# Performance work log

Measured on AMD Instinct MI355X. Metric: run time of the kernel, lower is better.

Reference implementation:

```python
import jax, jax.numpy as jnp
import numpy as np
import math

D_MODEL = 2048
N_HEADS = 16
D_K = D_MODEL // N_HEADS


def setup_inputs() -> dict:
    key = jax.random.key(0)
    ks = jax.random.split(key, 10)
    B, S = 1, 2048
    scale = 1.0 / math.sqrt(D_MODEL)
    x = jax.random.normal(ks[0], (B, S, D_MODEL), dtype=jnp.float32)
    mask = jnp.ones((1, 1, S, S), dtype=bool)
    Wq = jax.random.normal(ks[1], (D_MODEL, D_MODEL), dtype=jnp.float32) * scale
    bq = jnp.zeros((D_MODEL,), dtype=jnp.float32)
    Wk = jax.random.normal(ks[2], (D_MODEL, D_MODEL), dtype=jnp.float32) * scale
    bk = jnp.zeros((D_MODEL,), dtype=jnp.float32)
    Wv = jax.random.normal(ks[3], (D_MODEL, D_MODEL), dtype=jnp.float32) * scale
    bv = jnp.zeros((D_MODEL,), dtype=jnp.float32)
    Wo = jax.random.normal(ks[4], (D_MODEL, D_MODEL), dtype=jnp.float32) * scale
    bo = jnp.zeros((D_MODEL,), dtype=jnp.float32)
    return {"x": x, "mask": mask, "Wq": Wq, "bq": bq, "Wk": Wk, "bk": bk,
            "Wv": Wv, "bv": bv, "Wo": Wo, "bo": bo}


def reference(x, mask, Wq, bq, Wk, bk, Wv, bv, Wo, bo):
    B, S, D = x.shape
    # projections (nn.Linear: y = x @ W.T + b; here W stored as [in, out] so x @ W + b)
    def proj(W, b):
        y = x @ W + b                                   # [B, S, D]
        return y.reshape(B, S, N_HEADS, D_K).transpose(0, 2, 1, 3)  # [B, H, S, d_k]
    Q = proj(Wq, bq)
    K = proj(Wk, bk)
    V = proj(Wv, bv)
    scores = jnp.einsum('bhqd,bhkd->bhqk', Q, K) / math.sqrt(D_K)  # [B, H, S, S]
    scores = jnp.where(mask, scores, -jnp.inf)
    attn = jax.nn.softmax(scores, axis=-1)
    out = jnp.einsum('bhqk,bhkd->bhqd', attn, V)        # [B, H, S, d_k]
    out = out.transpose(0, 2, 1, 3).reshape(B, S, D)    # [B, S, D]
    return out @ Wo + bo
```

## Files before the change

kernel.cpp:

```cpp
#include <hip/hip_runtime.h>
#include <cstdint>
#include <cstddef>

typedef __bf16 bf16;
typedef bf16 bf16x8 __attribute__((ext_vector_type(8)));
typedef bf16 bf16x4 __attribute__((ext_vector_type(4)));
typedef bf16 bf16x2 __attribute__((ext_vector_type(2)));
typedef float f32x4 __attribute__((ext_vector_type(4)));
typedef float f32x16 __attribute__((ext_vector_type(16)));
typedef uint32_t u32x4 __attribute__((ext_vector_type(4)));

#define AS1 __attribute__((address_space(1)))
#define AS3 __attribute__((address_space(3)))

constexpr int DMODEL = 2048;
constexpr int SEQ    = 2048;
constexpr int DK     = 128;
constexpr float QSCALE_LOG2E = 0.12751740f;
constexpr float SM_SHIFT = 12.0f;

__global__ __launch_bounds__(256) void prep_kernel(
    const float* __restrict__ x, bf16* __restrict__ xb,
    const float* __restrict__ W0, const float* __restrict__ W1,
    const float* __restrict__ W2, const float* __restrict__ W3,
    bf16* __restrict__ T0, bf16* __restrict__ T1,
    bf16* __restrict__ T2, bf16* __restrict__ T3) {
  int bx = blockIdx.x;
  int tid = threadIdx.x;
  if (bx < 2048) {
    size_t i = (size_t)bx * 256 + tid;
    const float4 a = ((const float4*)x)[i * 2];
    const float4 b = ((const float4*)x)[i * 2 + 1];
    bf16x8 v;
    v[0] = (bf16)a.x; v[1] = (bf16)a.y; v[2] = (bf16)a.z; v[3] = (bf16)a.w;
    v[4] = (bf16)b.x; v[5] = (bf16)b.y; v[6] = (bf16)b.z; v[7] = (bf16)b.w;
    *(bf16x8*)(xb + i * 8) = v;
    return;
  }
  int b2 = bx - 2048;
  int z = b2 >> 10;
  int t = b2 & 1023;
  int bi = t >> 5, bj = t & 31;
  const float* W = (z == 0) ? W0 : (z == 1) ? W1 : (z == 2) ? W2 : W3;
  bf16* T        = (z == 0) ? T0 : (z == 1) ? T1 : (z == 2) ? T2 : T3;

  __shared__ float tile[64][68];
  int tr = tid >> 4, tc = tid & 15;
#pragma unroll
  for (int i = 0; i < 4; i++) {
    float4 v = *(const float4*)(W + (size_t)(bi * 64 + tr + i * 16) * DMODEL + bj * 64 + tc * 4);
    *(float4*)&tile[tr + i * 16][tc * 4] = v;
  }
  __syncthreads();
  int nl = tid >> 2, kc = (tid & 3) * 16;
  bf16x8 o0, o1;
#pragma unroll
  for (int j = 0; j < 8; j++) {
    o0[j] = (bf16)tile[kc + j][nl];
    o1[j] = (bf16)tile[kc + 8 + j][nl];
  }
  bf16* dst = T + (size_t)(bj * 64 + nl) * DMODEL + bi * 64 + kc;
  *(bf16x8*)dst       = o0;
  *(bf16x8*)(dst + 8) = o1;
}

__global__ __launch_bounds__(512, 2) void gemm256_qkv_kernel(
    const bf16* __restrict__ A,
    const bf16* __restrict__ Bt0, const float* __restrict__ bias0, bf16* __restrict__ outQ,
    const bf16* __restrict__ Bt1, const float* __restrict__ bias1, bf16* __restrict__ outK,
    const bf16* __restrict__ Bt2, const float* __restrict__ bias2, bf16* __restrict__ outV) {
  constexpr int NT = DMODEL / 64;
  __shared__ bf16 Asl[2][16384];
  __shared__ bf16 Bsl[2][16384];

  int zt = blockIdx.x >> 6;
  int t  = blockIdx.x & 63;
  int tm = t >> 3, tn = t & 7;
  int m0 = tm * 256, n0 = tn * 256;
  const bf16* Btp   = (zt == 0) ? Bt0 : (zt == 1) ? Bt1 : Bt2;
  const float* bias = (zt == 0) ? bias0 : (zt == 1) ? bias1 : bias2;

  int tid = threadIdx.x;
  int w = tid >> 6, l = tid & 63;
  int wm = w >> 2, wn = w & 3;
  int g = l >> 4, r16 = l & 15;

  int u0 = tid, u1 = 512 + tid;
  int r0 = u0 >> 3, s0 = u0 & 7;
  int r1 = u1 >> 3, s1 = u1 & 7;
  const bf16* aS0 = A + (size_t)(m0 + r0) * DMODEL + (s0 ^ (r0 & 7)) * 8;
  const bf16* aS1 = A + (size_t)(m0 + r1) * DMODEL + (s1 ^ (r1 & 7)) * 8;
  const bf16* bS0 = Btp + (size_t)(n0 + r0) * DMODEL + (s0 ^ (r0 & 7)) * 8;
  const bf16* bS1 = Btp + (size_t)(n0 + r1) * DMODEL + (s1 ^ (r1 & 7)) * 8;

  auto STAGE = [&](int tile, int h) {
    if (tile >= NT) return;
    int buf = tile & 1;
    size_t roff = (size_t)(h & 1) * 128 * DMODEL + (size_t)tile * 64;
    if (h < 2) {
      __builtin_amdgcn_global_load_lds((const AS1 void*)(aS0 + roff),
          (AS3 void*)(&Asl[buf][(h & 1) * 8192 + u0 * 8]), 16, 0, 0);
      __builtin_amdgcn_global_load_lds((const AS1 void*)(aS1 + roff),
          (AS3 void*)(&Asl[buf][(h & 1) * 8192 + u1 * 8]), 16, 0, 0);
    } else {
      __builtin_amdgcn_global_load_lds((const AS1 void*)(bS0 + roff),
          (AS3 void*)(&Bsl[buf][(h & 1) * 8192 + u0 * 8]), 16, 0, 0);
      __builtin_amdgcn_global_load_lds((const AS1 void*)(bS1 + roff),
          (AS3 void*)(&Bsl[buf][(h & 1) * 8192 + u1 * 8]), 16, 0, 0);
    }
  };

  bf16x8 afq[2][8];
  bf16x8 bfn[2][4];
  f32x4 acc[8][4];
#pragma unroll
  for (int i = 0; i < 8; i++)
#pragma unroll
    for (int j = 0; j < 4; j++) acc[i][j] = (f32x4){0.f, 0.f, 0.f, 0.f};

#define G256_LDA(MQ, BUF)                                                      \
  _Pragma("unroll")                                                            \
  for (int mf = 0; mf < 4; mf++) {                                             \
    int row = wm * 128 + (MQ) * 64 + mf * 16 + r16;                            \
    _Pragma("unroll")                                                          \
    for (int ks = 0; ks < 2; ks++)                                             \
      afq[MQ][mf * 2 + ks] =                                                   \
          *(const bf16x8*)(&Asl[BUF][row * 64 + (((ks * 4 + g) ^ (row & 7)) * 8)]); \
  }
#define G256_LDB(NQ, BUF)                                                      \
  _Pragma("unroll")                                                            \
  for (int nf = 0; nf < 2; nf++) {                                             \
    int row = wn * 64 + (NQ) * 32 + nf * 16 + r16;                             \
    _Pragma("unroll")                                                          \
    for (int ks = 0; ks < 2; ks++)                                             \
      bfn[NQ][nf * 2 + ks] =                                                   \
          *(const bf16x8*)(&Bsl[BUF][row * 64 + (((ks * 4 + g) ^ (row & 7)) * 8)]); \
  }
#define G256_MMA(MQ, NQ)                                                       \
  _Pragma("unroll")                                                            \
  for (int ks = 0; ks < 2; ks++)                                               \
    _Pragma("unroll")                                                          \
    for (int mf = 0; mf < 4; mf++)                                             \
      _Pragma("unroll")                                                        \
      for (int nf = 0; nf < 2; nf++)                                           \
        acc[(MQ) * 4 + mf][(NQ) * 2 + nf] =                                    \
            __builtin_amdgcn_mfma_f32_16x16x32_bf16(afq[MQ][mf * 2 + ks],      \
                bfn[NQ][nf * 2 + ks], acc[(MQ) * 4 + mf][(NQ) * 2 + nf], 0, 0, 0);
#define G256_BAR() __builtin_amdgcn_s_barrier()
#define G256_P1()  __builtin_amdgcn_s_setprio(1)
#define G256_P0()  __builtin_amdgcn_s_setprio(0)

  STAGE(0, 0); STAGE(0, 1); STAGE(0, 2); STAGE(0, 3);
  STAGE(1, 0); STAGE(1, 1); STAGE(1, 2);
  asm volatile("s_waitcnt vmcnt(6)" ::: "memory");
  G256_BAR();

  for (int it = 0; it < NT / 2; ++it) {
    int t1 = 2 * it + 1, t2 = 2 * it + 2, t3 = 2 * it + 3;
    G256_LDA(0, 0) G256_LDB(0, 0)
    STAGE(t1, 3);
    G256_BAR(); G256_P1(); G256_MMA(0, 0) G256_P0(); G256_BAR();
    G256_LDA(1, 0)
    STAGE(t2, 0);
    G256_BAR(); G256_P1(); G256_MMA(1, 0) G256_P0(); G256_BAR();
    G256_LDB(1, 0)
    STAGE(t2, 1);
    G256_BAR(); G256_P1(); G256_MMA(1, 1) G256_P0(); G256_BAR();
    STAGE(t2, 2);
    G256_BAR(); G256_P1(); G256_MMA(0, 1) G256_P0();
    if (it < NT / 2 - 1) asm volatile("s_waitcnt vmcnt(6)" ::: "memory");
    else                 asm volatile("s_waitcnt vmcnt(0)" ::: "memory");
    G256_BAR();
    G256_LDA(0, 1) G256_LDB(0, 1)
    STAGE(t2, 3);
    G256_BAR(); G256_P1(); G256_MMA(0, 0) G256_P0(); G256_BAR();
    G256_LDA(1, 1)
    STAGE(t3, 0);
    G256_BAR(); G256_P1(); G256_MMA(1, 0) G256_P0(); G256_BAR();
    G256_LDB(1, 1)
    STAGE(t3, 1);
    G256_BAR(); G256_P1(); G256_MMA(1, 1) G256_P0(); G256_BAR();
    STAGE(t3, 2);
    G256_BAR(); G256_P1(); G256_MMA(0, 1) G256_P0();
    if (it < NT / 2 - 1) asm volatile("s_waitcnt vmcnt(6)" ::: "memory");
    G256_BAR();
  }

  float bval[4];
#pragma unroll
  for (int nf = 0; nf < 4; nf++) bval[nf] = bias[n0 + wn * 64 + nf * 16 + r16];

  if (zt == 2) {
#pragma unroll
    for (int mf = 0; mf < 8; mf++)
#pragma unroll
      for (int nf = 0; nf < 4; nf++) {
        bf16x4 pk;
#pragma unroll
        for (int r = 0; r < 4; r++) pk[r] = (bf16)(acc[mf][nf][r] + bval[nf]);
        *(bf16x4*)(outV + (size_t)(n0 + wn * 64 + nf * 16 + r16) * SEQ +
                   m0 + wm * 128 + mf * 16 + g * 4) = pk;
      }
  } else {
    bf16* outp = (zt == 0) ? outQ : outK;
    float scl  = (zt == 0) ? QSCALE_LOG2E : 1.0f;
#pragma unroll
    for (int mf = 0; mf < 8; mf++)
#pragma unroll
      for (int nf = 0; nf < 4; nf++)
#pragma unroll
        for (int r = 0; r < 4; r++)
          outp[(size_t)(m0 + wm * 128 + mf * 16 + g * 4 + r) * DMODEL +
               n0 + wn * 64 + nf * 16 + r16] =
              (bf16)((acc[mf][nf][r] + bval[nf]) * scl);
  }
#undef G256_LDA
#undef G256_LDB
#undef G256_MMA
#undef G256_BAR
#undef G256_P1
#undef G256_P0
}

__global__ __launch_bounds__(256, 2) void attn_kernel(const bf16* __restrict__ Q,
                                                      const bf16* __restrict__ K,
                                                      const bf16* __restrict__ Vt,
                                                      bf16* __restrict__ Opart,
                                                      float* __restrict__ Lp) {
  constexpr int NT = 1024 / 64;
  int bx = blockIdx.x;
  int qt = bx >> 5;
  int hh = bx & 31;
  int h = hh >> 1, half = hh & 1;
  int tid = threadIdx.x;
  int w = tid >> 6, l = tid & 63;
  int q5 = l & 31, h5 = l >> 5;

  __shared__ bf16 KL[2][8192];
  __shared__ bf16 VL[2][8192];

  int q0 = qt * 128 + w * 32;

  const bf16* ksrc[4];
  const bf16* vsrc[4];
#pragma unroll
  for (int i = 0; i < 4; i++) {
    int unit = i * 256 + tid;
    ksrc[i] = K  + (size_t)(half * 1024 + (unit & 63)) * DMODEL + h * DK + (unit >> 6) * 8;
    vsrc[i] = Vt + (size_t)(h * DK + (unit & 127)) * SEQ + half * 1024 + (unit >> 7) * 8;
  }

#define ATTN_STAGE(BUF)                                                        \
  {                                                                            \
    _Pragma("unroll")                                                          \
    for (int i_ = 0; i_ < 4; i_++) {                                           \
      __builtin_amdgcn_global_load_lds((const AS1 void*)ksrc[i_],              \
          (AS3 void*)(&KL[BUF][(i_ * 256 + tid) * 8]), 16, 0, 0);              \
      ksrc[i_] += 64 * DMODEL;                                                 \
      __builtin_amdgcn_global_load_lds((const AS1 void*)vsrc[i_],              \
          (AS3 void*)(&VL[BUF][(i_ * 256 + tid) * 8]), 16, 0, 0);              \
      vsrc[i_] += 64;                                                          \
    }                                                                          \
  }

  bf16x8 qb[8];
  {
    const bf16* qbase = Q + (size_t)(q0 + q5) * DMODEL + h * DK + h5 * 8;
#pragma unroll
    for (int kc = 0; kc < 8; kc++) qb[kc] = *(const bf16x8*)(qbase + kc * 16);
  }

  f32x16 o[4];
#pragma unroll
  for (int vf = 0; vf < 4; vf++)
#pragma unroll
    for (int i = 0; i < 16; i++) o[vf][i] = 0.f;
  float lrow = 0.f;

  ATTN_STAGE(0);
  __syncthreads();

  for (int kb = 0; kb < NT; kb++) {
    int cur = kb & 1;
    if (kb + 1 < NT) ATTN_STAGE(cur ^ 1);

    const bf16* KB = &KL[cur][0];
    f32x16 s0, s1;
#pragma unroll
    for (int i = 0; i < 16; i++) { s0[i] = 0.f; s1[i] = 0.f; }
#pragma unroll
    for (int kc = 0; kc < 8; kc++) {
      bf16x8 k0 = *(const bf16x8*)(KB + ((kc * 2 + h5) * 64 + q5) * 8);
      bf16x8 k1 = *(const bf16x8*)(KB + ((kc * 2 + h5) * 64 + 32 + q5) * 8);
      s0 = __builtin_amdgcn_mfma_f32_32x32x16_bf16(k0, qb[kc], s0, 0, 0, 0);
      s1 = __builtin_amdgcn_mfma_f32_32x32x16_bf16(k1, qb[kc], s1, 0, 0, 0);
    }

#pragma unroll
    for (int i = 0; i < 16; i++) s0[i] = exp2f(s0[i] - SM_SHIFT);
#pragma unroll
    for (int i = 0; i < 16; i++) s1[i] = exp2f(s1[i] - SM_SHIFT);
    float ta[8];
#pragma unroll
    for (int i = 0; i < 8; i++) ta[i] = (s0[i] + s0[i + 8]) + (s1[i] + s1[i + 8]);
#pragma unroll
    for (int i = 0; i < 4; i++) ta[i] += ta[i + 4];
    float ps = (ta[0] + ta[2]) + (ta[1] + ta[3]);
    ps += __shfl_xor(ps, 32);
    lrow += ps;

    uint32_t u[16];
#pragma unroll
    for (int rp = 0; rp < 8; rp++) {
      bf16x2 t0; t0[0] = (bf16)s0[2 * rp]; t0[1] = (bf16)s0[2 * rp + 1];
      u[rp] = __builtin_bit_cast(uint32_t, t0);
      bf16x2 t1; t1[0] = (bf16)s1[2 * rp]; t1[1] = (bf16)s1[2 * rp + 1];
      u[8 + rp] = __builtin_bit_cast(uint32_t, t1);
    }
#pragma unroll
    for (int b = 0; b < 16; b += 4) {
      asm volatile("v_permlane32_swap_b32 %0, %1" : "+v"(u[b]),     "+v"(u[b + 2]));
      asm volatile("v_permlane32_swap_b32 %0, %1" : "+v"(u[b + 1]), "+v"(u[b + 3]));
    }

    const bf16* VB = &VL[cur][0];
#pragma unroll
    for (int ks = 0; ks < 4; ks++) {
      u32x4 tw = {u[ks * 4], u[ks * 4 + 1], u[ks * 4 + 2], u[ks * 4 + 3]};
      bf16x8 pb = __builtin_bit_cast(bf16x8, tw);
#pragma unroll
      for (int vf = 0; vf < 4; vf++) {
        bf16x8 vv = *(const bf16x8*)(VB + ((ks * 2 + h5) * 128 + vf * 32 + q5) * 8);
        o[vf] = __builtin_amdgcn_mfma_f32_32x32x16_bf16(vv, pb, o[vf], 0, 0, 0);
      }
    }
    __syncthreads();
  }

  bf16* obase = Opart + ((size_t)hh * SEQ + q0 + q5) * DK + h5 * 4;
#pragma unroll
  for (int vf = 0; vf < 4; vf++)
#pragma unroll
    for (int rr = 0; rr < 4; rr++) {
      bf16x4 pk;
#pragma unroll
      for (int c = 0; c < 4; c++) pk[c] = (bf16)o[vf][rr * 4 + c];
      *(bf16x4*)(obase + vf * 32 + rr * 8) = pk;
    }
  if (h5 == 0) Lp[(size_t)hh * SEQ + q0 + q5] = lrow;
#undef ATTN_STAGE
}

__global__ __launch_bounds__(256) void attn_merge_kernel(const bf16* __restrict__ Opart,
                                                         const float* __restrict__ Lp,
                                                         bf16* __restrict__ AO) {
  size_t idx = (size_t)blockIdx.x * 256 + threadIdx.x;
  int d8 = idx & 15;
  int q  = (int)((idx >> 4) & 2047);
  int h  = (int)(idx >> 15);
  size_t ra = (size_t)(h * 2) * SEQ + q;
  size_t rb = (size_t)(h * 2 + 1) * SEQ + q;
  float inv = 1.0f / (Lp[ra] + Lp[rb]);
  bf16x8 a = *(const bf16x8*)(Opart + ra * DK + d8 * 8);
  bf16x8 b = *(const bf16x8*)(Opart + rb * DK + d8 * 8);
  bf16x8 r;
#pragma unroll
  for (int j = 0; j < 8; j++)
    r[j] = (bf16)(((float)a[j] + (float)b[j]) * inv);
  *(bf16x8*)(AO + (size_t)q * DMODEL + h * DK + d8 * 8) = r;
}

__global__ __launch_bounds__(256) void gemm_bt_kernel(
    const bf16* __restrict__ A,
    const bf16* __restrict__ Btp, const float* __restrict__ bias,
    float* __restrict__ outF) {
  __shared__ bf16 Als[128 * 64];
  __shared__ bf16 Bls[128 * 64];

  int t = blockIdx.x;
  int tm = t >> 4, tn = t & 15;
  int m0 = tm * 128, n0 = tn * 128;
  int tid = threadIdx.x;
  int w = tid >> 6, l = tid & 63;
  int wm = w >> 1, wn = w & 1;
  int g = l >> 4, r16 = l & 15;

  f32x4 acc[4][4];
#pragma unroll
  for (int i = 0; i < 4; i++)
#pragma unroll
    for (int j = 0; j < 4; j++) acc[i][j] = (f32x4){0.f, 0.f, 0.f, 0.f};

  int lrow = l >> 3;
  for (int kt = 0; kt < DMODEL / 64; kt++) {
    const bf16* abase = A   + (size_t)m0 * DMODEL + kt * 64;
    const bf16* bbase = Btp + (size_t)n0 * DMODEL + kt * 64;
#pragma unroll
    for (int i = 0; i < 4; i++) {
      int chunk = w * 4 + i;
      int row   = chunk * 8 + lrow;
      int slot  = (l & 7) ^ (row & 7);
      __builtin_amdgcn_global_load_lds((const AS1 void*)(abase + (size_t)row * DMODEL + slot * 8),
                                       (AS3 void*)(Als + chunk * 512), 16, 0, 0);
      __builtin_amdgcn_global_load_lds((const AS1 void*)(bbase + (size_t)row * DMODEL + slot * 8),
                                       (AS3 void*)(Bls + chunk * 512), 16, 0, 0);
    }
    __syncthreads();
#pragma unroll
    for (int ks = 0; ks < 2; ks++) {
      bf16x8 af[4], bfr[4];
#pragma unroll
      for (int mf = 0; mf < 4; mf++) {
        int row  = wm * 64 + mf * 16 + r16;
        int slot = (ks * 4 + g) ^ (row & 7);
        af[mf] = *(const bf16x8*)(Als + row * 64 + slot * 8);
      }
#pragma unroll
      for (int nf = 0; nf < 4; nf++) {
        int row  = wn * 64 + nf * 16 + r16;
        int slot = (ks * 4 + g) ^ (row & 7);
        bfr[nf] = *(const bf16x8*)(Bls + row * 64 + slot * 8);
      }
#pragma unroll
      for (int mf = 0; mf < 4; mf++)
#pragma unroll
        for (int nf = 0; nf < 4; nf++)
          acc[mf][nf] = __builtin_amdgcn_mfma_f32_16x16x32_bf16(af[mf], bfr[nf], acc[mf][nf], 0, 0, 0);
    }
    __syncthreads();
  }

  float bval[4];
#pragma unroll
  for (int nf = 0; nf < 4; nf++) bval[nf] = bias[n0 + wn * 64 + nf * 16 + r16];
#pragma unroll
  for (int mf = 0; mf < 4; mf++)
#pragma unroll
    for (int nf = 0; nf < 4; nf++)
#pragma unroll
      for (int r = 0; r < 4; r++)
        outF[(size_t)(m0 + wm * 64 + mf * 16 + g * 4 + r) * DMODEL + n0 + wn * 64 + nf * 16 + r16] =
            acc[mf][nf][r] + bval[nf];
}

extern "C" void kernel_launch(void* const* d_in, const int* in_sizes, int n_in,
                              void* d_out, int out_size, void* d_ws, size_t ws_size,
                              hipStream_t stream) {
  const float* x  = (const float*)d_in[0];
  const float* Wq = (const float*)d_in[2];
  const float* bq = (const float*)d_in[3];
  const float* Wk = (const float*)d_in[4];
  const float* bk = (const float*)d_in[5];
  const float* Wv = (const float*)d_in[6];
  const float* bv = (const float*)d_in[7];
  const float* Wo = (const float*)d_in[8];
  const float* bo = (const float*)d_in[9];
  float* out = (float*)d_out;

  const size_t MAT = (size_t)DMODEL * DMODEL;
  bf16* p   = (bf16*)d_ws;
  bf16* xb  = p; p += MAT;
  bf16* Wqt = p; p += MAT;
  bf16* Wkt = p; p += MAT;
  bf16* Wvt = p; p += MAT;
  bf16* Wot = p; p += MAT;
  bf16* Qb  = p; p += MAT;
  bf16* Kb  = p; p += MAT;
  bf16* Vtb = p; p += MAT;
  bf16* AOb = p; p += MAT;
  bf16* Opart  = xb;
  float* Lpart = (float*)p;

  prep_kernel<<<6144, 256, 0, stream>>>(x, xb, Wq, Wk, Wv, Wo, Wqt, Wkt, Wvt, Wot);
  gemm256_qkv_kernel<<<192, 512, 0, stream>>>(xb, Wqt, bq, Qb, Wkt, bk, Kb, Wvt, bv, Vtb);
  attn_kernel<<<512, 256, 0, stream>>>(Qb, Kb, Vtb, Opart, Lpart);
  attn_merge_kernel<<<2048, 256, 0, stream>>>(Opart, Lpart, AOb);
  gemm_bt_kernel<<<256, 256, 0, stream>>>(AOb, Wot, bo, out);
}
```

Measured before the change: 182.9 us.

## Fuse QKV projections into one GEMM with 256x192 tiles over concatenated weights

Replaces the three-way z-split QKV GEMM (192 blocks of 256x256) with a single GEMM over the concatenated transposed Q/K/V weights (N=6144), tiled 256x192, giving 256 blocks. That count fills the 256 CUs evenly in one wave, where 192 blocks left some idle. The load and MMA schedule is rebuilt for the narrower B tile, and the epilogue picks the bias and output per column. It relies on Wqt/Wkt/Wvt sitting contiguously in the workspace, which the layout provides, and the new vmcnt waits must match the changed load counts.

```diff
diff --git a/kernel.cpp b/kernel.cpp
--- a/kernel.cpp
+++ b/kernel.cpp
@@ -64,21 +64,18 @@
   *(bf16x8*)(dst + 8) = o1;
 }
 
-__global__ __launch_bounds__(512, 2) void gemm256_qkv_kernel(
+__global__ __launch_bounds__(512, 2) void gemm_qkv_fused_kernel(
     const bf16* __restrict__ A,
-    const bf16* __restrict__ Bt0, const float* __restrict__ bias0, bf16* __restrict__ outQ,
-    const bf16* __restrict__ Bt1, const float* __restrict__ bias1, bf16* __restrict__ outK,
-    const bf16* __restrict__ Bt2, const float* __restrict__ bias2, bf16* __restrict__ outV) {
+    const bf16* __restrict__ BtF,
+    const float* __restrict__ bias0, const float* __restrict__ bias1,
+    const float* __restrict__ bias2,
+    bf16* __restrict__ outQ, bf16* __restrict__ outK, bf16* __restrict__ outV) {
   constexpr int NT = DMODEL / 64;
   __shared__ bf16 Asl[2][16384];
-  __shared__ bf16 Bsl[2][16384];
-
-  int zt = blockIdx.x >> 6;
-  int t  = blockIdx.x & 63;
-  int tm = t >> 3, tn = t & 7;
-  int m0 = tm * 256, n0 = tn * 256;
-  const bf16* Btp   = (zt == 0) ? Bt0 : (zt == 1) ? Bt1 : Bt2;
-  const float* bias = (zt == 0) ? bias0 : (zt == 1) ? bias1 : bias2;
+  __shared__ bf16 Bsl[2][12288];
+
+  int tm = blockIdx.x >> 5, tn = blockIdx.x & 31;
+  int m0 = tm * 256, n0 = tn * 192;
 
   int tid = threadIdx.x;
   int w = tid >> 6, l = tid & 63;
@@ -90,35 +87,35 @@
   int r1 = u1 >> 3, s1 = u1 & 7;
   const bf16* aS0 = A + (size_t)(m0 + r0) * DMODEL + (s0 ^ (r0 & 7)) * 8;
   const bf16* aS1 = A + (size_t)(m0 + r1) * DMODEL + (s1 ^ (r1 & 7)) * 8;
-  const bf16* bS0 = Btp + (size_t)(n0 + r0) * DMODEL + (s0 ^ (r0 & 7)) * 8;
-  const bf16* bS1 = Btp + (size_t)(n0 + r1) * DMODEL + (s1 ^ (r1 & 7)) * 8;
-
-  auto STAGE = [&](int tile, int h) {
+  int br = tid >> 3, bs = tid & 7;
+  const bf16* bS = BtF + (size_t)(n0 + br) * DMODEL + (bs ^ (br & 7)) * 8;
+
+  auto STAGE_A = [&](int tile, int h) {
     if (tile >= NT) return;
     int buf = tile & 1;
-    size_t roff = (size_t)(h & 1) * 128 * DMODEL + (size_t)tile * 64;
-    if (h < 2) {
-      __builtin_amdgcn_global_load_lds((const AS1 void*)(aS0 + roff),
-          (AS3 void*)(&Asl[buf][(h & 1) * 8192 + u0 * 8]), 16, 0, 0);
-      __builtin_amdgcn_global_load_lds((const AS1 void*)(aS1 + roff),
-          (AS3 void*)(&Asl[buf][(h & 1) * 8192 + u1 * 8]), 16, 0, 0);
-    } else {
-      __builtin_amdgcn_global_load_lds((const AS1 void*)(bS0 + roff),
-          (AS3 void*)(&Bsl[buf][(h & 1) * 8192 + u0 * 8]), 16, 0, 0);
-      __builtin_amdgcn_global_load_lds((const AS1 void*)(bS1 + roff),
-          (AS3 void*)(&Bsl[buf][(h & 1) * 8192 + u1 * 8]), 16, 0, 0);
-    }
+    size_t roff = (size_t)h * 128 * DMODEL + (size_t)tile * 64;
+    __builtin_amdgcn_global_load_lds((const AS1 void*)(aS0 + roff),
+        (AS3 void*)(&Asl[buf][h * 8192 + u0 * 8]), 16, 0, 0);
+    __builtin_amdgcn_global_load_lds((const AS1 void*)(aS1 + roff),
+        (AS3 void*)(&Asl[buf][h * 8192 + u1 * 8]), 16, 0, 0);
   };
+  auto STAGE_B = [&](int tile, int gb) {
+    if (tile >= NT) return;
+    int buf = tile & 1;
+    __builtin_amdgcn_global_load_lds(
+        (const AS1 void*)(bS + (size_t)gb * 64 * DMODEL + (size_t)tile * 64),
+        (AS3 void*)(&Bsl[buf][(gb * 512 + tid) * 8]), 16, 0, 0);
+  };
 
   bf16x8 afq[2][8];
-  bf16x8 bfn[2][4];
-  f32x4 acc[8][4];
+  bf16x8 bfn[3][2];
+  f32x4 acc[8][3];
 #pragma unroll
   for (int i = 0; i < 8; i++)
 #pragma unroll
-    for (int j = 0; j < 4; j++) acc[i][j] = (f32x4){0.f, 0.f, 0.f, 0.f};
-
-#define G256_LDA(MQ, BUF)                                                      \
+    for (int j = 0; j < 3; j++) acc[i][j] = (f32x4){0.f, 0.f, 0.f, 0.f};
+
+#define GF_LDA(MQ, BUF)                                                        \
   _Pragma("unroll")                                                            \
   for (int mf = 0; mf < 4; mf++) {                                             \
     int row = wm * 128 + (MQ) * 64 + mf * 16 + r16;                            \
@@ -127,99 +124,113 @@
       afq[MQ][mf * 2 + ks] =                                                   \
           *(const bf16x8*)(&Asl[BUF][row * 64 + (((ks * 4 + g) ^ (row & 7)) * 8)]); \
   }
-#define G256_LDB(NQ, BUF)                                                      \
+#define GF_LDB01(BUF)                                                          \
   _Pragma("unroll")                                                            \
   for (int nf = 0; nf < 2; nf++) {                                             \
-    int row = wn * 64 + (NQ) * 32 + nf * 16 + r16;                             \
+    int row = wn * 48 + nf * 16 + r16;                                         \
     _Pragma("unroll")                                                          \
     for (int ks = 0; ks < 2; ks++)                                             \
-      bfn[NQ][nf * 2 + ks] =                                                   \
+      bfn[nf][ks] =                                                            \
           *(const bf16x8*)(&Bsl[BUF][row * 64 + (((ks * 4 + g) ^ (row & 7)) * 8)]); \
   }
-#define G256_MMA(MQ, NQ)                                                       \
+#define GF_LDB2(BUF)                                                           \
+  {                                                                            \
+    int row = wn * 48 + 32 + r16;                                              \
+    _Pragma("unroll")                                                          \
+    for (int ks = 0; ks < 2; ks++)                                             \
+      bfn[2][ks] =                                                             \
+          *(const bf16x8*)(&Bsl[BUF][row * 64 + (((ks * 4 + g) ^ (row & 7)) * 8)]); \
+  }
+#define GF_MMA01(MQ)                                                           \
   _Pragma("unroll")                                                            \
   for (int ks = 0; ks < 2; ks++)                                               \
     _Pragma("unroll")                                                          \
     for (int mf = 0; mf < 4; mf++)                                             \
       _Pragma("unroll")                                                        \
       for (int nf = 0; nf < 2; nf++)                                           \
-        acc[(MQ) * 4 + mf][(NQ) * 2 + nf] =                                    \
+        acc[(MQ) * 4 + mf][nf] =                                               \
             __builtin_amdgcn_mfma_f32_16x16x32_bf16(afq[MQ][mf * 2 + ks],      \
-                bfn[NQ][nf * 2 + ks], acc[(MQ) * 4 + mf][(NQ) * 2 + nf], 0, 0, 0);
-#define G256_BAR() __builtin_amdgcn_s_barrier()
-#define G256_P1()  __builtin_amdgcn_s_setprio(1)
-#define G256_P0()  __builtin_amdgcn_s_setprio(0)
-
-  STAGE(0, 0); STAGE(0, 1); STAGE(0, 2); STAGE(0, 3);
-  STAGE(1, 0); STAGE(1, 1); STAGE(1, 2);
-  asm volatile("s_waitcnt vmcnt(6)" ::: "memory");
-  G256_BAR();
+                bfn[nf][ks], acc[(MQ) * 4 + mf][nf], 0, 0, 0);
+#define GF_MMA2()                                                              \
+  _Pragma("unroll")                                                            \
+  for (int ks = 0; ks < 2; ks++)                                               \
+    _Pragma("unroll")                                                          \
+    for (int mq = 0; mq < 2; mq++)                                             \
+      _Pragma("unroll")                                                        \
+      for (int mf = 0; mf < 4; mf++)                                           \
+        acc[mq * 4 + mf][2] =                                                  \
+            __builtin_amdgcn_mfma_f32_16x16x32_bf16(afq[mq][mf * 2 + ks],      \
+                bfn[2][ks], acc[mq * 4 + mf][2], 0, 0, 0);
+#define GF_BAR() __builtin_amdgcn_s_barrier()
+#define GF_P1()  __builtin_amdgcn_s_setprio(1)
+#define GF_P0()  __builtin_amdgcn_s_setprio(0)
+
+  STAGE_A(0, 0); STAGE_A(0, 1);
+  STAGE_B(0, 0); STAGE_B(0, 1); STAGE_B(0, 2);
+  STAGE_A(1, 0); STAGE_A(1, 1);
+  asm volatile("s_waitcnt vmcnt(4)" ::: "memory");
+  GF_BAR();
 
   for (int it = 0; it < NT / 2; ++it) {
     int t1 = 2 * it + 1, t2 = 2 * it + 2, t3 = 2 * it + 3;
-    G256_LDA(0, 0) G256_LDB(0, 0)
-    STAGE(t1, 3);
-    G256_BAR(); G256_P1(); G256_MMA(0, 0) G256_P0(); G256_BAR();
-    G256_LDA(1, 0)
-    STAGE(t2, 0);
-    G256_BAR(); G256_P1(); G256_MMA(1, 0) G256_P0(); G256_BAR();
-    G256_LDB(1, 0)
-    STAGE(t2, 1);
-    G256_BAR(); G256_P1(); G256_MMA(1, 1) G256_P0(); G256_BAR();
-    STAGE(t2, 2);
-    G256_BAR(); G256_P1(); G256_MMA(0, 1) G256_P0();
-    if (it < NT / 2 - 1) asm volatile("s_waitcnt vmcnt(6)" ::: "memory");
+    GF_LDA(0, 0) GF_LDB01(0)
+    STAGE_B(t1, 0); STAGE_B(t1, 1); STAGE_B(t1, 2);
+    GF_BAR(); GF_P1(); GF_MMA01(0) GF_P0(); GF_BAR();
+    GF_LDA(1, 0)
+    GF_BAR(); GF_P1(); GF_MMA01(1) GF_P0(); GF_BAR();
+    GF_LDB2(0)
+    STAGE_A(t2, 0);
+    GF_BAR(); GF_P1(); GF_MMA2() GF_P0();
+    if (it < NT / 2 - 1) asm volatile("s_waitcnt vmcnt(2)" ::: "memory");
     else                 asm volatile("s_waitcnt vmcnt(0)" ::: "memory");
-    G256_BAR();
-    G256_LDA(0, 1) G256_LDB(0, 1)
-    STAGE(t2, 3);
-    G256_BAR(); G256_P1(); G256_MMA(0, 0) G256_P0(); G256_BAR();
-    G256_LDA(1, 1)
-    STAGE(t3, 0);
-    G256_BAR(); G256_P1(); G256_MMA(1, 0) G256_P0(); G256_BAR();
-    G256_LDB(1, 1)
-    STAGE(t3, 1);
-    G256_BAR(); G256_P1(); G256_MMA(1, 1) G256_P0(); G256_BAR();
-    STAGE(t3, 2);
-    G256_BAR(); G256_P1(); G256_MMA(0, 1) G256_P0();
-    if (it < NT / 2 - 1) asm volatile("s_waitcnt vmcnt(6)" ::: "memory");
-    G256_BAR();
-  }
-
-  float bval[4];
-#pragma unroll
-  for (int nf = 0; nf < 4; nf++) bval[nf] = bias[n0 + wn * 64 + nf * 16 + r16];
-
-  if (zt == 2) {
-#pragma unroll
-    for (int mf = 0; mf < 8; mf++)
-#pragma unroll
-      for (int nf = 0; nf < 4; nf++) {
+    GF_BAR();
+    GF_LDA(0, 1) GF_LDB01(1)
+    STAGE_A(t2, 1);
+    GF_BAR(); GF_P1(); GF_MMA01(0) GF_P0(); GF_BAR();
+    GF_LDA(1, 1)
+    STAGE_B(t2, 0); STAGE_B(t2, 1);
+    GF_BAR(); GF_P1(); GF_MMA01(1) GF_P0(); GF_BAR();
+    GF_LDB2(1)
+    STAGE_B(t2, 2); STAGE_A(t3, 0); STAGE_A(t3, 1);
+    GF_BAR(); GF_P1(); GF_MMA2() GF_P0();
+    if (it < NT / 2 - 1) asm volatile("s_waitcnt vmcnt(4)" ::: "memory");
+    GF_BAR();
+  }
+
+#pragma unroll
+  for (int nf = 0; nf < 3; nf++) {
+    int col  = n0 + wn * 48 + nf * 16 + r16;
+    int ztf  = col >> 11;
+    int lcol = col & 2047;
+    const float* bp = (ztf == 0) ? bias0 : (ztf == 1) ? bias1 : bias2;
+    float bval = bp[lcol];
+    if (ztf == 2) {
+#pragma unroll
+      for (int mf = 0; mf < 8; mf++) {
         bf16x4 pk;
 #pragma unroll
-        for (int r = 0; r < 4; r++) pk[r] = (bf16)(acc[mf][nf][r] + bval[nf]);
-        *(bf16x4*)(outV + (size_t)(n0 + wn * 64 + nf * 16 + r16) * SEQ +
-                   m0 + wm * 128 + mf * 16 + g * 4) = pk;
+        for (int r = 0; r < 4; r++) pk[r] = (bf16)(acc[mf][nf][r] + bval);
+        *(bf16x4*)(outV + (size_t)lcol * SEQ + m0 + wm * 128 + mf * 16 + g * 4) = pk;
       }
-  } else {
-    bf16* outp = (zt == 0) ? outQ : outK;
-    float scl  = (zt == 0) ? QSCALE_LOG2E : 1.0f;
-#pragma unroll
-    for (int mf = 0; mf < 8; mf++)
-#pragma unroll
-      for (int nf = 0; nf < 4; nf++)
+    } else {
+      bf16* outp = (ztf == 0) ? outQ : outK;
+      float scl  = (ztf == 0) ? QSCALE_LOG2E : 1.0f;
+#pragma unroll
+      for (int mf = 0; mf < 8; mf++)
 #pragma unroll
         for (int r = 0; r < 4; r++)
-          outp[(size_t)(m0 + wm * 128 + mf * 16 + g * 4 + r) * DMODEL +
-               n0 + wn * 64 + nf * 16 + r16] =
-              (bf16)((acc[mf][nf][r] + bval[nf]) * scl);
-  }
-#undef G256_LDA
-#undef G256_LDB
-#undef G256_MMA
-#undef G256_BAR
-#undef G256_P1
-#undef G256_P0
+          outp[(size_t)(m0 + wm * 128 + mf * 16 + g * 4 + r) * DMODEL + lcol] =
+              (bf16)((acc[mf][nf][r] + bval) * scl);
+    }
+  }
+#undef GF_LDA
+#undef GF_LDB01
+#undef GF_LDB2
+#undef GF_MMA01
+#undef GF_MMA2
+#undef GF_BAR
+#undef GF_P1
+#undef GF_P0
 }
 
 __global__ __launch_bounds__(256, 2) void attn_kernel(const bf16* __restrict__ Q,
@@ -472,7 +483,7 @@
   float* Lpart = (float*)p;
 
   prep_kernel<<<6144, 256, 0, stream>>>(x, xb, Wq, Wk, Wv, Wo, Wqt, Wkt, Wvt, Wot);
-  gemm256_qkv_kernel<<<192, 512, 0, stream>>>(xb, Wqt, bq, Qb, Wkt, bk, Kb, Wvt, bv, Vtb);
+  gemm_qkv_fused_kernel<<<256, 512, 0, stream>>>(xb, Wqt, bq, bk, bv, Qb, Kb, Vtb);
   attn_kernel<<<512, 256, 0, stream>>>(Qb, Kb, Vtb, Opart, Lpart);
   attn_merge_kernel<<<2048, 256, 0, stream>>>(Opart, Lpart, AOb);
   gemm_bt_kernel<<<256, 256, 0, stream>>>(AOb, Wot, bo, out);
```

Measured after the change: 176.3 us (median of 3 runs). 3.6% less time.
